# Kernel optimization log

Hardware: AMD Instinct MI355X
Metric: run time of the kernel (lower is better)

Reference implementation:

```python
import jax, jax.numpy as jnp
import numpy as np

IN_FEATURES = 256
OUT_FEATURES = 128
K = 2
KK = 2 ** K
TABLES = IN_FEATURES * OUT_FEATURES
BATCH = 256


def _build_input_mask():
    # Faithful port of _input_mask_builder: per output, random indices with
    # every k-th entry forced to arange(in_features).
    rng = np.random.RandomState(0)
    rows = []
    for _ in range(OUT_FEATURES):
        idx = rng.choice(IN_FEATURES, IN_FEATURES * K)
        idx[::K] = np.arange(IN_FEATURES)
        rows.append(idx)
    return jnp.asarray(np.asarray(rows).flatten(), dtype=jnp.int64)


def setup_inputs() -> dict:
    key = jax.random.key(0)
    k1, k2, k3 = jax.random.split(key, 3)
    return {
        "input": jax.random.normal(k1, (BATCH, IN_FEATURES), dtype=jnp.float32),
        "weight": jax.random.normal(k2, (TABLES, KK), dtype=jnp.float32),
        "bias": jax.random.normal(k3, (OUT_FEATURES,), dtype=jnp.float32),
        "input_mask": _build_input_mask(),
    }


def reference(input, weight, bias, input_mask):
    # Truth table vertices in {-1,+1}: (K, KK)
    tt = ((((jnp.arange(KK)[None, :] >> jnp.arange(K)[:, None]) & 1) * 2 - 1)
          ).astype(input.dtype)
    B = input.shape[0]
    x = input[:, input_mask].reshape(B, TABLES, K)           # gather
    # Lagrange interpolation: prod_k (1 + x_k * v_k)/2 -> (B, T, KK)
    red = jnp.prod((1.0 + x[..., None] * tt) * 0.5, axis=2)
    out = jnp.einsum("btc,tc->bt", red, weight)              # per-table LUT
    out = out.reshape(B, OUT_FEATURES, IN_FEATURES).sum(-1)  # segment reduce
    return out + bias
```

## Files before the change

### kernel.cpp

```cpp
#include <hip/hip_runtime.h>
#include <stdint.h>


#define IN_F   256
#define OUT_F  128
#define B_TILE 64
#define NW     8
#define TPW    32

__global__ __launch_bounds__(256) void prep_kernel(
    const float* __restrict__ weight,
    const int*   __restrict__ mask32,
    const float* __restrict__ bias,
    float4*      __restrict__ pk,
    float*       __restrict__ bias2)
{
    __shared__ float wsum[IN_F];
    __shared__ float ared[IN_F];
    const int o = blockIdx.x;
    const int i = threadIdx.x;
    const int t = o * IN_F + i;

    int probe = 0;
    #pragma unroll
    for (int k = 1; k < 32; k += 2) probe |= mask32[k];
    const bool is64 = (probe == 0);

    float4 w = ((const float4*)weight)[t];
    float s01 = w.x + w.y, s23 = w.z + w.w;
    float d01 = w.y - w.x, d23 = w.w - w.z;
    float A = 0.25f * (s01 + s23);
    float B = 0.25f * (d01 + d23);
    float C = 0.25f * (s23 - s01);
    float D = 0.25f * (d23 - d01);
    int m1 = mask32[is64 ? (4 * t + 2) : (2 * t + 1)];

    wsum[i] = B;
    ared[i] = A;
    __syncthreads();
    atomicAdd(&wsum[m1], C);
    __syncthreads();

    float4 r;
    r.x = wsum[i];
    r.y = D;
    r.z = __int_as_float(m1 << 8);
    r.w = __int_as_float((((m1 >> 2) & 31)) << 2);
    pk[t] = r;

    #pragma unroll
    for (int s = 128; s > 0; s >>= 1) {
        if (i < s) ared[i] += ared[i + s];
        __syncthreads();
    }
    if (i == 0) bias2[o] = bias[o] + ared[0];
}

__global__ __launch_bounds__(512, 4) void lut_linear_kernel(
    const float*  __restrict__ input,
    const float4* __restrict__ pk,
    const float*  __restrict__ bias2,
    float*        __restrict__ out)
{
    __shared__ float  ldsT[IN_F * B_TILE];
    __shared__ float4 pkl[IN_F];
    __shared__ float  pt[NW][B_TILE];

    const int tid  = threadIdx.x;
    const int o    = blockIdx.x >> 2;
    const int b0   = (blockIdx.x & 3) * B_TILE;
    const int lane = tid & 63;
    const int w    = __builtin_amdgcn_readfirstlane(tid >> 6);

    if (tid < IN_F) pkl[tid] = pk[o * IN_F + tid];

    const float4* in4 = (const float4*)(input + (size_t)b0 * IN_F);
    #pragma unroll
    for (int it = 0; it < 8; ++it) {
        int idx4 = it * 512 + tid;
        float4 v = in4[idx4];
        int g = idx4 << 2;
        int b = g >> 8;
        int f = g & 255;
        int bb = b ^ ((f >> 2) & 31);
        ldsT[f * 64 + bb]       = v.x;
        ldsT[(f + 1) * 64 + bb] = v.y;
        ldsT[(f + 2) * 64 + bb] = v.z;
        ldsT[(f + 3) * 64 + bb] = v.w;
    }
    __syncthreads();

    const int   Lw    = lane ^ ((w & 3) << 3);
    const int   lane4 = lane << 2;
    const float* xbase = ldsT + w * (TPW * 64);
    const char*  ldsB  = (const char*)ldsT;

    float acc = 0.0f;
    #pragma unroll
    for (int j = 0; j < TPW; ++j) {
        float4 c = pkl[w * TPW + j];
        int woff = __float_as_int(c.z);
        int s4   = __float_as_int(c.w);
        float x1 = *(const float*)(ldsB + woff + (lane4 ^ s4));
        float x0 = xbase[j * 64 + (Lw ^ (j >> 2))];
        acc = fmaf(x0, fmaf(c.y, x1, c.x), acc);
    }

    pt[w][lane] = acc;
    __syncthreads();

    if (tid < B_TILE) {
        float r = 0.0f;
        #pragma unroll
        for (int k = 0; k < NW; ++k) r += pt[k][tid];
        out[(size_t)(b0 + tid) * OUT_F + o] = r + bias2[o];
    }
}

extern "C" void kernel_launch(void* const* d_in, const int* in_sizes, int n_in,
                              void* d_out, int out_size, void* d_ws, size_t ws_size,
                              hipStream_t stream) {
    const float* input  = (const float*)d_in[0];
    const float* weight = (const float*)d_in[1];
    const float* bias   = (const float*)d_in[2];
    const int*   mask32 = (const int*)d_in[3];
    float* out = (float*)d_out;

    float4* pk    = (float4*)d_ws;
    float*  bias2 = (float*)((char*)d_ws + 32768 * sizeof(float4));

    prep_kernel<<<dim3(OUT_F), dim3(256), 0, stream>>>(weight, mask32, bias, pk, bias2);
    lut_linear_kernel<<<dim3(OUT_F * 4), dim3(512), 0, stream>>>(input, pk, bias2, out);
}
```

Baseline: 65.96 us.

## Fuse weight preprocessing into main LUT kernel, drop separate prep launch

Moves the per-output weight transform (Lagrange coefficients, mask-indexed atomic scatter, bias reduction) into the main kernel so each block computes its own packed coefficients in LDS. This removes a second kernel launch and the global round trip through the workspace. Each output's prep work is now repeated by its 4 batch-tile blocks. The swizzle offset is also folded into a single XOR key, saving an integer op per gather.

New measurement: 65.10 us. About the same (-1.3%).

```diff
diff --git a/kernel.cpp b/kernel.cpp
--- a/kernel.cpp
+++ b/kernel.cpp
@@ -8,71 +8,24 @@
 #define NW     8
 #define TPW    32
 
-__global__ __launch_bounds__(256) void prep_kernel(
+__global__ __launch_bounds__(512, 4) void lut_linear_fused(
+    const float* __restrict__ input,
     const float* __restrict__ weight,
+    const float* __restrict__ bias,
     const int*   __restrict__ mask32,
-    const float* __restrict__ bias,
-    float4*      __restrict__ pk,
-    float*       __restrict__ bias2)
-{
-    __shared__ float wsum[IN_F];
-    __shared__ float ared[IN_F];
-    const int o = blockIdx.x;
-    const int i = threadIdx.x;
-    const int t = o * IN_F + i;
-
-    int probe = 0;
-    #pragma unroll
-    for (int k = 1; k < 32; k += 2) probe |= mask32[k];
-    const bool is64 = (probe == 0);
-
-    float4 w = ((const float4*)weight)[t];
-    float s01 = w.x + w.y, s23 = w.z + w.w;
-    float d01 = w.y - w.x, d23 = w.w - w.z;
-    float A = 0.25f * (s01 + s23);
-    float B = 0.25f * (d01 + d23);
-    float C = 0.25f * (s23 - s01);
-    float D = 0.25f * (d23 - d01);
-    int m1 = mask32[is64 ? (4 * t + 2) : (2 * t + 1)];
-
-    wsum[i] = B;
-    ared[i] = A;
-    __syncthreads();
-    atomicAdd(&wsum[m1], C);
-    __syncthreads();
-
-    float4 r;
-    r.x = wsum[i];
-    r.y = D;
-    r.z = __int_as_float(m1 << 8);
-    r.w = __int_as_float((((m1 >> 2) & 31)) << 2);
-    pk[t] = r;
-
-    #pragma unroll
-    for (int s = 128; s > 0; s >>= 1) {
-        if (i < s) ared[i] += ared[i + s];
-        __syncthreads();
-    }
-    if (i == 0) bias2[o] = bias[o] + ared[0];
-}
-
-__global__ __launch_bounds__(512, 4) void lut_linear_kernel(
-    const float*  __restrict__ input,
-    const float4* __restrict__ pk,
-    const float*  __restrict__ bias2,
-    float*        __restrict__ out)
+    float*       __restrict__ out)
 {
     __shared__ float  ldsT[IN_F * B_TILE];
     __shared__ float4 pkl[IN_F];
+    __shared__ float  wsum[IN_F];
     __shared__ float  pt[NW][B_TILE];
+    __shared__ float  asum[8];
 
     const int tid  = threadIdx.x;
     const int o    = blockIdx.x >> 2;
     const int b0   = (blockIdx.x & 3) * B_TILE;
     const int lane = tid & 63;
     const int w    = __builtin_amdgcn_readfirstlane(tid >> 6);
-
-    if (tid < IN_F) pkl[tid] = pk[o * IN_F + tid];
 
     const float4* in4 = (const float4*)(input + (size_t)b0 * IN_F);
     #pragma unroll
@@ -88,10 +41,46 @@
         ldsT[(f + 2) * 64 + bb] = v.z;
         ldsT[(f + 3) * 64 + bb] = v.w;
     }
+
+    float Av = 0.0f, Cv = 0.0f, Dv = 0.0f;
+    int   Kv = 0, m1 = 0;
+    if (tid < IN_F) {
+        int probe = 0;
+        #pragma unroll
+        for (int k = 1; k < 32; k += 2) probe |= mask32[k];
+        const bool is64 = (probe == 0);
+
+        const int t = o * IN_F + tid;
+        float4 wq = ((const float4*)weight)[t];
+        float s01 = wq.x + wq.y, s23 = wq.z + wq.w;
+        float d01 = wq.y - wq.x, d23 = wq.w - wq.z;
+        Av = 0.25f * (s01 + s23);
+        float Bv = 0.25f * (d01 + d23);
+        Cv = 0.25f * (s23 - s01);
+        Dv = 0.25f * (d23 - d01);
+        m1 = mask32[is64 ? (4 * t + 2) : (2 * t + 1)];
+        Kv = (m1 << 8) ^ ((((m1 >> 2) & 31)) << 2);
+        wsum[tid] = Bv;
+    }
     __syncthreads();
 
-    const int   Lw    = lane ^ ((w & 3) << 3);
-    const int   lane4 = lane << 2;
+    if (tid < IN_F) {
+        atomicAdd(&wsum[m1], Cv);
+        #pragma unroll
+        for (int off = 32; off > 0; off >>= 1)
+            Av += __shfl_down(Av, off, 64);
+        if (lane == 0) asum[w] = Av;
+    }
+    __syncthreads();
+
+    if (tid < IN_F)
+        pkl[tid] = make_float4(wsum[tid], Dv, __int_as_float(Kv), 0.0f);
+    if (tid == 0)
+        asum[4] = bias[o] + asum[0] + asum[1] + asum[2] + asum[3];
+    __syncthreads();
+
+    const int    Lw    = lane ^ ((w & 3) << 3);
+    const int    lane4 = lane << 2;
     const float* xbase = ldsT + w * (TPW * 64);
     const char*  ldsB  = (const char*)ldsT;
 
@@ -99,9 +88,7 @@
     #pragma unroll
     for (int j = 0; j < TPW; ++j) {
         float4 c = pkl[w * TPW + j];
-        int woff = __float_as_int(c.z);
-        int s4   = __float_as_int(c.w);
-        float x1 = *(const float*)(ldsB + woff + (lane4 ^ s4));
+        float x1 = *(const float*)(ldsB + (__float_as_int(c.z) ^ lane4));
         float x0 = xbase[j * 64 + (Lw ^ (j >> 2))];
         acc = fmaf(x0, fmaf(c.y, x1, c.x), acc);
     }
@@ -110,10 +97,10 @@
     __syncthreads();
 
     if (tid < B_TILE) {
-        float r = 0.0f;
+        float r = asum[4];
         #pragma unroll
         for (int k = 0; k < NW; ++k) r += pt[k][tid];
-        out[(size_t)(b0 + tid) * OUT_F + o] = r + bias2[o];
+        out[(size_t)(b0 + tid) * OUT_F + o] = r;
     }
 }
 
@@ -126,9 +113,6 @@
     const int*   mask32 = (const int*)d_in[3];
     float* out = (float*)d_out;
 
-    float4* pk    = (float4*)d_ws;
-    float*  bias2 = (float*)((char*)d_ws + 32768 * sizeof(float4));
-
-    prep_kernel<<<dim3(OUT_F), dim3(256), 0, stream>>>(weight, mask32, bias, pk, bias2);
-    lut_linear_kernel<<<dim3(OUT_F * 4), dim3(512), 0, stream>>>(input, pk, bias2, out);
+    lut_linear_fused<<<dim3(OUT_F * 4), dim3(512), 0, stream>>>(
+        input, weight, bias, mask32, out);
 }
```
